# Optimization experiments

Hardware: AMD Instinct MI355X
Metric: run time of the kernel (lower is better)

The kernel has to match this reference:

```python
import jax, jax.numpy as jnp
import numpy as np
from jax.scipy.special import logsumexp

N_STATES = 512
N_OBS = 1024
BATCH = 64
T_MAX = 512


def setup_inputs() -> dict:
    key = jax.random.key(0)
    k1, k2, k3, k4, k5 = jax.random.split(key, 5)
    pi = jnp.zeros((N_STATES,), dtype=jnp.float32)
    A = jax.random.normal(k1, (N_STATES, N_STATES), dtype=jnp.float32)  # unnormalized transition
    E = jax.random.normal(k2, (N_STATES, N_OBS), dtype=jnp.float32)     # unnormalized emission
    x = jax.random.randint(k3, (BATCH, T_MAX), 0, N_OBS)
    T = jax.random.randint(k4, (BATCH,), 1, T_MAX + 1)
    return {"pi": pi, "A": A, "E": E, "x": x, "T": T}


def reference(pi, A, E, x, T):
    # log p(x) via forward algorithm in log domain.
    log_pi = jax.nn.log_softmax(pi)                # (N,)
    log_A = jax.nn.log_softmax(A, axis=0)          # (N,N), matches torch dim=0
    log_E = jax.nn.log_softmax(E, axis=1)          # (N,M)

    # emission log-probs per timestep: (B, T_max, N)
    log_em = jnp.moveaxis(log_E[:, x], 0, -1)

    alpha0 = log_em[:, 0, :] + log_pi              # (B,N)

    def step(carry, em_t):
        # carry: (B,N) over k; log_A: (N_i, N_k)
        # next[b,i] = em_t[b,i] + logsumexp_k(log_A[i,k] + carry[b,k])
        nxt = em_t + logsumexp(log_A[None, :, :] + carry[:, None, :], axis=2)
        return nxt, nxt

    em_rest = jnp.swapaxes(log_em[:, 1:, :], 0, 1)  # (T_max-1, B, N)
    _, alphas = jax.lax.scan(step, alpha0, em_rest)
    log_alpha = jnp.concatenate([alpha0[:, None, :], jnp.swapaxes(alphas, 0, 1)], axis=1)  # (B,T_max,N)

    log_sums = logsumexp(log_alpha, axis=2)         # (B, T_max)
    log_probs = jnp.take_along_axis(log_sums, (T - 1)[:, None], axis=1)  # (B,1)
    return log_probs
```

## Files before the change

kernel.cpp:

```cpp
#include <hip/hip_runtime.h>
#include <math.h>

#define NS   512
#define NO   1024
#define NB   64
#define TMAX 512

#define QREG 50
#define QLDS 14

typedef _Float16 h2v __attribute__((ext_vector_type(2)));

__device__ inline float wave_red_sum(float x) {
#pragma unroll
  for (int o = 32; o; o >>= 1) x += __shfl_xor(x, o, 64);
  return x;
}
__device__ inline float wave_red_max(float x) {
#pragma unroll
  for (int o = 32; o; o >>= 1) x = fmaxf(x, __shfl_xor(x, o, 64));
  return x;
}

__device__ inline float dot2u(unsigned int a, unsigned int b, float c) {
#if __has_builtin(__builtin_amdgcn_fdot2)
  return __builtin_amdgcn_fdot2(__builtin_bit_cast(h2v, a),
                                __builtin_bit_cast(h2v, b), c, false);
#else
  h2v av = __builtin_bit_cast(h2v, a), bv = __builtin_bit_cast(h2v, b);
  return c + (float)av.x * (float)bv.x + (float)av.y * (float)bv.y;
#endif
}

__global__ void k_pi(const float* __restrict__ pi, float* __restrict__ pi_sm) {
  __shared__ float red[8];
  int tid = threadIdx.x;
  float v = pi[tid];
  float m = wave_red_max(v);
  if ((tid & 63) == 0) red[tid >> 6] = m;
  __syncthreads();
  m = fmaxf(fmaxf(fmaxf(red[0], red[1]), fmaxf(red[2], red[3])),
            fmaxf(fmaxf(red[4], red[5]), fmaxf(red[6], red[7])));
  float e = __expf(v - m);
  float s = wave_red_sum(e);
  __syncthreads();
  if ((tid & 63) == 0) red[tid >> 6] = s;
  __syncthreads();
  s = red[0] + red[1] + red[2] + red[3] + red[4] + red[5] + red[6] + red[7];
  pi_sm[tid] = e / s;
}

__global__ void k_colLse(const float* __restrict__ A, float* __restrict__ lseA) {
  __shared__ float redm[4];
  __shared__ float reds[4];
  int k = blockIdx.x, tid = threadIdx.x;
  float a0 = A[tid * NS + k], a1 = A[(tid + 256) * NS + k];
  float m = wave_red_max(fmaxf(a0, a1));
  if ((tid & 63) == 0) redm[tid >> 6] = m;
  __syncthreads();
  m = fmaxf(fmaxf(redm[0], redm[1]), fmaxf(redm[2], redm[3]));
  float s = __expf(a0 - m) + __expf(a1 - m);
  s = wave_red_sum(s);
  if ((tid & 63) == 0) reds[tid >> 6] = s;
  __syncthreads();
  s = reds[0] + reds[1] + reds[2] + reds[3];
  if (tid == 0) lseA[k] = m + __logf(s);
}

__global__ void k_rowLseE(const float* __restrict__ E, float* __restrict__ lseE) {
  __shared__ float red[4];
  int i = blockIdx.x, tid = threadIdx.x;
  const float* row = E + i * NO;
  float a0 = row[tid], a1 = row[tid + 256], a2 = row[tid + 512], a3 = row[tid + 768];
  float m = fmaxf(fmaxf(a0, a1), fmaxf(a2, a3));
  m = wave_red_max(m);
  if ((tid & 63) == 0) red[tid >> 6] = m;
  __syncthreads();
  m = fmaxf(fmaxf(red[0], red[1]), fmaxf(red[2], red[3]));
  float s = __expf(a0 - m) + __expf(a1 - m) + __expf(a2 - m) + __expf(a3 - m);
  s = wave_red_sum(s);
  __syncthreads();
  if ((tid & 63) == 0) red[tid >> 6] = s;
  __syncthreads();
  s = red[0] + red[1] + red[2] + red[3];
  if (tid == 0) lseE[i] = m + __logf(s);
}

__global__ void k_pack(const float* __restrict__ A, const float* __restrict__ lseA,
                       unsigned int* __restrict__ W) {
  int u = blockIdx.x * 512 + threadIdx.x;
  int h = u & 3;
  int ct = u >> 2;
  int t = ct & 511;
  int c = ct >> 9;
  int j = c >> 3, m = c & 7;
  int w = t >> 6, l = t & 63;
  int i  = 64 * j + l;
  int k0 = 64 * w + 8 * m + 2 * h;
  float e0 = __expf(A[i * NS + k0]     - lseA[k0]);
  float e1 = __expf(A[i * NS + k0 + 1] - lseA[k0 + 1]);
  h2v p;
  p.x = (_Float16)e0;
  p.y = (_Float16)e1;
  W[u] = __builtin_bit_cast(unsigned int, p);
}

__global__ __launch_bounds__(512, 1) void k_fwd(
    const float* __restrict__ E, const int* __restrict__ x,
    const int* __restrict__ Tlen, const float* __restrict__ pi_sm,
    const float* __restrict__ lseE, const uint4* __restrict__ Apk,
    float* __restrict__ out) {
  __shared__ uint4 Alds[QLDS * 512];
  __shared__ float Pf[2][8 * 512];
  __shared__ uint4 ubuf[NS / 8];
  __shared__ int xrow[TMAX];
  __shared__ __align__(16) float red[2][8];
  int b = blockIdx.x, tid = threadIdx.x;
  int w = tid >> 6, l = tid & 63;

  uint4 areg[QREG];
#pragma unroll
  for (int q = 0; q < QREG; q++) areg[q] = Apk[q * 512 + tid];
#pragma unroll
  for (int q = 0; q < QLDS; q++) Alds[q * 512 + tid] = Apk[(QREG + q) * 512 + tid];

  for (int t2 = tid; t2 < TMAX; t2 += 512) xrow[t2] = x[b * TMAX + t2];

  float pi_i  = pi_sm[tid];
  float lse_i = lseE[tid];
  const float* Erow = E + tid * NO;
  int Tb = Tlen[b];
  float c = 0.f;
  float Dlog = 0.f;
  int gexp_prev = 19;
  int cur = 0;
  __syncthreads();

  for (int t = 0; t < Tb; t++) {
    int nxt = cur ^ 1;
    float epre = Erow[xrow[t]];
    if (t) {
      uint4 uv0 = ubuf[8 * w + 0], uv1 = ubuf[8 * w + 1];
      uint4 uv2 = ubuf[8 * w + 2], uv3 = ubuf[8 * w + 3];
      uint4 uv4 = ubuf[8 * w + 4], uv5 = ubuf[8 * w + 5];
      uint4 uv6 = ubuf[8 * w + 6], uv7 = ubuf[8 * w + 7];
      float acc[8];
#pragma unroll
      for (int j = 0; j < 8; j++) acc[j] = 0.f;
#pragma unroll
      for (int j = 0; j < 8; j++) {
#pragma unroll
        for (int m = 0; m < 8; m++) {
          int cq = j * 8 + m;
          uint4 av = (cq < QREG) ? areg[cq] : Alds[(cq - QREG) * 512 + tid];
          uint4 uv = (m == 0) ? uv0 : (m == 1) ? uv1 : (m == 2) ? uv2 :
                     (m == 3) ? uv3 : (m == 4) ? uv4 : (m == 5) ? uv5 :
                     (m == 6) ? uv6 : uv7;
          acc[j] = dot2u(av.x, uv.x, acc[j]);
          acc[j] = dot2u(av.y, uv.y, acc[j]);
          acc[j] = dot2u(av.z, uv.z, acc[j]);
          acc[j] = dot2u(av.w, uv.w, acc[j]);
        }
      }
#pragma unroll
      for (int j = 0; j < 8; j++) Pf[cur][w * 512 + j * 64 + l] = acc[j];
    }
    __syncthreads();

    {
      int gexpw = 19;
      if (t) {
        const float4* rp = (const float4*)red[cur];
        float4 ra = rp[0], rb = rp[1];
        float sp = ((ra.x + ra.y) + (ra.z + ra.w)) + ((rb.x + rb.y) + (rb.z + rb.w));
        float ls = __log2f(sp);
        int e = ((__builtin_bit_cast(int, sp) >> 23) & 0xff) - 126;
        c += ls - Dlog;
        Dlog = (float)gexp_prev + ls;
        gexpw = 19 - gexp_prev - e;
      }
      float em = __expf(epre - lse_i);
      float raw;
      if (t) {
        const float* pf = Pf[cur];
        float s0 = pf[tid]          + pf[512 + tid];
        float s1 = pf[1024 + tid]   + pf[1536 + tid];
        float s2 = pf[2048 + tid]   + pf[2560 + tid];
        float s3 = pf[3072 + tid]   + pf[3584 + tid];
        raw = ((s0 + s1) + (s2 + s3)) * em;
      } else {
        raw = pi_i * em;
      }
      ((_Float16*)ubuf)[tid] = (_Float16)ldexpf(raw, gexpw);
      float s = wave_red_sum(raw);
      if (l == 0) red[nxt][w] = s;
      gexp_prev = gexpw;
    }
    cur = nxt;
  }
  __syncthreads();
  {
    const float4* rp = (const float4*)red[cur];
    float4 ra = rp[0], rb = rp[1];
    float sp = ((ra.x + ra.y) + (ra.z + ra.w)) + ((rb.x + rb.y) + (rb.z + rb.w));
    c += __log2f(sp) - Dlog;
  }
  if (tid == 0) out[b] = c * 0.69314718055994530942f;
}

extern "C" void kernel_launch(void* const* d_in, const int* in_sizes, int n_in,
                              void* d_out, int out_size, void* d_ws, size_t ws_size,
                              hipStream_t stream) {
  const float* pi = (const float*)d_in[0];
  const float* A  = (const float*)d_in[1];
  const float* E  = (const float*)d_in[2];
  const int*   x  = (const int*)d_in[3];
  const int*   T  = (const int*)d_in[4];
  float* out = (float*)d_out;

  char* ws = (char*)d_ws;
  float*        pi_sm = (float*)(ws + 0);
  float*        lseA  = (float*)(ws + 2048);
  float*        lseE  = (float*)(ws + 4096);
  unsigned int* Apk   = (unsigned int*)(ws + 6144);

  hipLaunchKernelGGL(k_pi,      dim3(1),   dim3(512), 0, stream, pi, pi_sm);
  hipLaunchKernelGGL(k_colLse,  dim3(512), dim3(256), 0, stream, A, lseA);
  hipLaunchKernelGGL(k_rowLseE, dim3(512), dim3(256), 0, stream, E, lseE);
  hipLaunchKernelGGL(k_pack,    dim3(256), dim3(512), 0, stream, A, lseA, Apk);
  hipLaunchKernelGGL(k_fwd,     dim3(64),  dim3(512), 0, stream,
                     E, x, T, pi_sm, lseE, (const uint4*)Apk, out);
}
```

Measured before the change: 833.3 us.

## Store transition matrix as FP8 e5m2 and expand to fp16 for dot2

Packs the normalized transition probabilities into 8-bit e5m2 (scaled by 256) instead of fp16, halving the per-block storage of A so that fewer uint4s are held in registers and LDS. In the forward loop each byte pair is expanded to fp16 with a byte permute before the fdot2, and the 1/256 scale is folded into the emission multiply. This trades a couple of extra ALU ops per dot for reduced register pressure and LDS traffic, at the cost of much coarser precision (2-bit mantissa) on the transition weights, which may hurt accuracy.

```diff
diff --git a/kernel.cpp b/kernel.cpp
--- a/kernel.cpp
+++ b/kernel.cpp
@@ -6,8 +6,8 @@
 #define NB   64
 #define TMAX 512
 
-#define QREG 50
-#define QLDS 14
+#define QREG8 19
+#define QLDS8 13
 
 typedef _Float16 h2v __attribute__((ext_vector_type(2)));
 
@@ -32,6 +32,27 @@
 #endif
 }
 
+__device__ inline unsigned int ex_lo(unsigned int w) {
+#if __has_builtin(__builtin_amdgcn_perm)
+  return __builtin_amdgcn_perm(0u, w, 0x010C000Cu);
+#else
+  return ((w & 0xFFu) << 8) | ((w & 0xFF00u) << 16);
+#endif
+}
+__device__ inline unsigned int ex_hi(unsigned int w) {
+#if __has_builtin(__builtin_amdgcn_perm)
+  return __builtin_amdgcn_perm(0u, w, 0x030C020Cu);
+#else
+  return ((w & 0x00FF0000u) >> 8) | (w & 0xFF000000u);
+#endif
+}
+
+__device__ inline unsigned int f2e5m2(float f) {
+  unsigned short hb = __builtin_bit_cast(unsigned short, (_Float16)f);
+  unsigned int r = (unsigned int)hb + 0x7Fu + ((hb >> 8) & 1u);
+  return (r >> 8) & 0xFFu;
+}
+
 __global__ void k_pi(const float* __restrict__ pi, float* __restrict__ pi_sm) {
   __shared__ float red[8];
   int tid = threadIdx.x;
@@ -92,17 +113,17 @@
   int h = u & 3;
   int ct = u >> 2;
   int t = ct & 511;
-  int c = ct >> 9;
-  int j = c >> 3, m = c & 7;
+  int c8 = ct >> 9;
+  int j = c8 >> 2, n = c8 & 3;
   int w = t >> 6, l = t & 63;
   int i  = 64 * j + l;
-  int k0 = 64 * w + 8 * m + 2 * h;
-  float e0 = __expf(A[i * NS + k0]     - lseA[k0]);
-  float e1 = __expf(A[i * NS + k0 + 1] - lseA[k0 + 1]);
-  h2v p;
-  p.x = (_Float16)e0;
-  p.y = (_Float16)e1;
-  W[u] = __builtin_bit_cast(unsigned int, p);
+  int k0 = 64 * w + 16 * n + 4 * h;
+  const float* row = A + i * NS;
+  unsigned int b0 = f2e5m2(__expf(row[k0]     - lseA[k0])     * 256.f);
+  unsigned int b1 = f2e5m2(__expf(row[k0 + 1] - lseA[k0 + 1]) * 256.f);
+  unsigned int b2 = f2e5m2(__expf(row[k0 + 2] - lseA[k0 + 2]) * 256.f);
+  unsigned int b3 = f2e5m2(__expf(row[k0 + 3] - lseA[k0 + 3]) * 256.f);
+  W[u] = b0 | (b1 << 8) | (b2 << 16) | (b3 << 24);
 }
 
 __global__ __launch_bounds__(512, 1) void k_fwd(
@@ -110,7 +131,7 @@
     const int* __restrict__ Tlen, const float* __restrict__ pi_sm,
     const float* __restrict__ lseE, const uint4* __restrict__ Apk,
     float* __restrict__ out) {
-  __shared__ uint4 Alds[QLDS * 512];
+  __shared__ uint4 Alds[QLDS8 * 512];
   __shared__ float Pf[2][8 * 512];
   __shared__ uint4 ubuf[NS / 8];
   __shared__ int xrow[TMAX];
@@ -118,11 +139,11 @@
   int b = blockIdx.x, tid = threadIdx.x;
   int w = tid >> 6, l = tid & 63;
 
-  uint4 areg[QREG];
-#pragma unroll
-  for (int q = 0; q < QREG; q++) areg[q] = Apk[q * 512 + tid];
-#pragma unroll
-  for (int q = 0; q < QLDS; q++) Alds[q * 512 + tid] = Apk[(QREG + q) * 512 + tid];
+  uint4 areg8[QREG8];
+#pragma unroll
+  for (int q = 0; q < QREG8; q++) areg8[q] = Apk[q * 512 + tid];
+#pragma unroll
+  for (int q = 0; q < QLDS8; q++) Alds[q * 512 + tid] = Apk[(QREG8 + q) * 512 + tid];
 
   for (int t2 = tid; t2 < TMAX; t2 += 512) xrow[t2] = x[b * TMAX + t2];
 
@@ -140,26 +161,29 @@
     int nxt = cur ^ 1;
     float epre = Erow[xrow[t]];
     if (t) {
-      uint4 uv0 = ubuf[8 * w + 0], uv1 = ubuf[8 * w + 1];
-      uint4 uv2 = ubuf[8 * w + 2], uv3 = ubuf[8 * w + 3];
-      uint4 uv4 = ubuf[8 * w + 4], uv5 = ubuf[8 * w + 5];
-      uint4 uv6 = ubuf[8 * w + 6], uv7 = ubuf[8 * w + 7];
+      uint4 uvA0 = ubuf[8 * w + 0], uvB0 = ubuf[8 * w + 1];
+      uint4 uvA1 = ubuf[8 * w + 2], uvB1 = ubuf[8 * w + 3];
+      uint4 uvA2 = ubuf[8 * w + 4], uvB2 = ubuf[8 * w + 5];
+      uint4 uvA3 = ubuf[8 * w + 6], uvB3 = ubuf[8 * w + 7];
       float acc[8];
 #pragma unroll
       for (int j = 0; j < 8; j++) acc[j] = 0.f;
 #pragma unroll
       for (int j = 0; j < 8; j++) {
 #pragma unroll
-        for (int m = 0; m < 8; m++) {
-          int cq = j * 8 + m;
-          uint4 av = (cq < QREG) ? areg[cq] : Alds[(cq - QREG) * 512 + tid];
-          uint4 uv = (m == 0) ? uv0 : (m == 1) ? uv1 : (m == 2) ? uv2 :
-                     (m == 3) ? uv3 : (m == 4) ? uv4 : (m == 5) ? uv5 :
-                     (m == 6) ? uv6 : uv7;
-          acc[j] = dot2u(av.x, uv.x, acc[j]);
-          acc[j] = dot2u(av.y, uv.y, acc[j]);
-          acc[j] = dot2u(av.z, uv.z, acc[j]);
-          acc[j] = dot2u(av.w, uv.w, acc[j]);
+        for (int n = 0; n < 4; n++) {
+          int c8 = j * 4 + n;
+          uint4 av = (c8 < QREG8) ? areg8[c8] : Alds[(c8 - QREG8) * 512 + tid];
+          uint4 uvA = (n == 0) ? uvA0 : (n == 1) ? uvA1 : (n == 2) ? uvA2 : uvA3;
+          uint4 uvB = (n == 0) ? uvB0 : (n == 1) ? uvB1 : (n == 2) ? uvB2 : uvB3;
+          acc[j] = dot2u(ex_lo(av.x), uvA.x, acc[j]);
+          acc[j] = dot2u(ex_hi(av.x), uvA.y, acc[j]);
+          acc[j] = dot2u(ex_lo(av.y), uvA.z, acc[j]);
+          acc[j] = dot2u(ex_hi(av.y), uvA.w, acc[j]);
+          acc[j] = dot2u(ex_lo(av.z), uvB.x, acc[j]);
+          acc[j] = dot2u(ex_hi(av.z), uvB.y, acc[j]);
+          acc[j] = dot2u(ex_lo(av.w), uvB.z, acc[j]);
+          acc[j] = dot2u(ex_hi(av.w), uvB.w, acc[j]);
         }
       }
 #pragma unroll
@@ -187,7 +211,7 @@
         float s1 = pf[1024 + tid]   + pf[1536 + tid];
         float s2 = pf[2048 + tid]   + pf[2560 + tid];
         float s3 = pf[3072 + tid]   + pf[3584 + tid];
-        raw = ((s0 + s1) + (s2 + s3)) * em;
+        raw = ((s0 + s1) + (s2 + s3)) * (em * 0.00390625f);
       } else {
         raw = pi_i * em;
       }
@@ -227,7 +251,7 @@
   hipLaunchKernelGGL(k_pi,      dim3(1),   dim3(512), 0, stream, pi, pi_sm);
   hipLaunchKernelGGL(k_colLse,  dim3(512), dim3(256), 0, stream, A, lseA);
   hipLaunchKernelGGL(k_rowLseE, dim3(512), dim3(256), 0, stream, E, lseE);
-  hipLaunchKernelGGL(k_pack,    dim3(256), dim3(512), 0, stream, A, lseA, Apk);
+  hipLaunchKernelGGL(k_pack,    dim3(128), dim3(512), 0, stream, A, lseA, Apk);
   hipLaunchKernelGGL(k_fwd,     dim3(64),  dim3(512), 0, stream,
                      E, x, T, pi_sm, lseE, (const uint4*)Apk, out);
 }
```

Measured after the change: 1.063 ms. 27.6% more time.

## Double threads per batch block in forward recursion and halve per-thread K slice

Applied to the files above, without the earlier changes.

The forward-kernel block grows from 512 to 1024 threads. Each wave now covers a 32-wide slice of the previous-state dimension instead of 64, so each thread's register and LDS share of the packed transition matrix halves and the dot-product chain per step is shorter. Partial sums go through LDS as packed fp16 pairs. Only half the lanes own a state for the emission, normalisation and reduction phase. This is meant to cut the serial per-step latency, at the cost of fp16 rounding in the partial sums, idle lanes in the epilogue and heavier barriers.

```diff
diff --git a/kernel.cpp b/kernel.cpp
--- a/kernel.cpp
+++ b/kernel.cpp
@@ -6,8 +6,8 @@
 #define NB   64
 #define TMAX 512
 
-#define QREG 50
-#define QLDS 14
+#define QREG 25
+#define QLDS 7
 
 typedef _Float16 h2v __attribute__((ext_vector_type(2)));
 
@@ -91,12 +91,12 @@
   int u = blockIdx.x * 512 + threadIdx.x;
   int h = u & 3;
   int ct = u >> 2;
-  int t = ct & 511;
-  int c = ct >> 9;
-  int j = c >> 3, m = c & 7;
+  int t = ct & 1023;
+  int c = ct >> 10;
+  int j = c >> 2, n = c & 3;
   int w = t >> 6, l = t & 63;
   int i  = 64 * j + l;
-  int k0 = 64 * w + 8 * m + 2 * h;
+  int k0 = 32 * w + 8 * n + 2 * h;
   float e0 = __expf(A[i * NS + k0]     - lseA[k0]);
   float e1 = __expf(A[i * NS + k0 + 1] - lseA[k0 + 1]);
   h2v p;
@@ -105,30 +105,37 @@
   W[u] = __builtin_bit_cast(unsigned int, p);
 }
 
-__global__ __launch_bounds__(512, 1) void k_fwd(
+__global__ __launch_bounds__(1024, 1) void k_fwd(
     const float* __restrict__ E, const int* __restrict__ x,
     const int* __restrict__ Tlen, const float* __restrict__ pi_sm,
     const float* __restrict__ lseE, const uint4* __restrict__ Apk,
     float* __restrict__ out) {
-  __shared__ uint4 Alds[QLDS * 512];
-  __shared__ float Pf[2][8 * 512];
-  __shared__ uint4 ubuf[NS / 8];
+  __shared__ uint4 Alds[QLDS * 1024];
+  __shared__ unsigned int Pf[2][8 * 512];
+  __shared__ __align__(16) uint4 ubuf[NS / 8];
   __shared__ int xrow[TMAX];
-  __shared__ __align__(16) float red[2][8];
+  __shared__ __align__(16) float red[2][16];
   int b = blockIdx.x, tid = threadIdx.x;
   int w = tid >> 6, l = tid & 63;
+  int lo = l & 31;
+  bool owner = (l < 32);
+  int i_own = 32 * w + lo;
 
   uint4 areg[QREG];
 #pragma unroll
-  for (int q = 0; q < QREG; q++) areg[q] = Apk[q * 512 + tid];
-#pragma unroll
-  for (int q = 0; q < QLDS; q++) Alds[q * 512 + tid] = Apk[(QREG + q) * 512 + tid];
-
-  for (int t2 = tid; t2 < TMAX; t2 += 512) xrow[t2] = x[b * TMAX + t2];
-
-  float pi_i  = pi_sm[tid];
-  float lse_i = lseE[tid];
-  const float* Erow = E + tid * NO;
+  for (int q = 0; q < QREG; q++) areg[q] = Apk[q * 1024 + tid];
+#pragma unroll
+  for (int q = 0; q < QLDS; q++) Alds[q * 1024 + tid] = Apk[(QREG + q) * 1024 + tid];
+
+  for (int t2 = tid; t2 < TMAX; t2 += 1024) xrow[t2] = x[b * TMAX + t2];
+
+  float pi_i = 0.f, lse_i = 0.f;
+  const float* Erow = E;
+  if (owner) {
+    pi_i  = pi_sm[i_own];
+    lse_i = lseE[i_own];
+    Erow  = E + i_own * NO;
+  }
   int Tb = Tlen[b];
   float c = 0.f;
   float Dlog = 0.f;
@@ -138,32 +145,30 @@
 
   for (int t = 0; t < Tb; t++) {
     int nxt = cur ^ 1;
-    float epre = Erow[xrow[t]];
+    float epre = owner ? Erow[xrow[t]] : 0.f;
     if (t) {
-      uint4 uv0 = ubuf[8 * w + 0], uv1 = ubuf[8 * w + 1];
-      uint4 uv2 = ubuf[8 * w + 2], uv3 = ubuf[8 * w + 3];
-      uint4 uv4 = ubuf[8 * w + 4], uv5 = ubuf[8 * w + 5];
-      uint4 uv6 = ubuf[8 * w + 6], uv7 = ubuf[8 * w + 7];
+      uint4 uv0 = ubuf[4 * w + 0], uv1 = ubuf[4 * w + 1];
+      uint4 uv2 = ubuf[4 * w + 2], uv3 = ubuf[4 * w + 3];
       float acc[8];
 #pragma unroll
       for (int j = 0; j < 8; j++) acc[j] = 0.f;
 #pragma unroll
       for (int j = 0; j < 8; j++) {
 #pragma unroll
-        for (int m = 0; m < 8; m++) {
-          int cq = j * 8 + m;
-          uint4 av = (cq < QREG) ? areg[cq] : Alds[(cq - QREG) * 512 + tid];
-          uint4 uv = (m == 0) ? uv0 : (m == 1) ? uv1 : (m == 2) ? uv2 :
-                     (m == 3) ? uv3 : (m == 4) ? uv4 : (m == 5) ? uv5 :
-                     (m == 6) ? uv6 : uv7;
+        for (int n = 0; n < 4; n++) {
+          int cq = j * 4 + n;
+          uint4 av = (cq < QREG) ? areg[cq] : Alds[(cq - QREG) * 1024 + tid];
+          uint4 uv = (n == 0) ? uv0 : (n == 1) ? uv1 : (n == 2) ? uv2 : uv3;
           acc[j] = dot2u(av.x, uv.x, acc[j]);
           acc[j] = dot2u(av.y, uv.y, acc[j]);
           acc[j] = dot2u(av.z, uv.z, acc[j]);
           acc[j] = dot2u(av.w, uv.w, acc[j]);
         }
       }
-#pragma unroll
-      for (int j = 0; j < 8; j++) Pf[cur][w * 512 + j * 64 + l] = acc[j];
+      _Float16* pfh = (_Float16*)Pf[cur];
+#pragma unroll
+      for (int j = 0; j < 8; j++)
+        pfh[(((w >> 1) * 512 + 64 * j + l) << 1) | (w & 1)] = (_Float16)acc[j];
     }
     __syncthreads();
 
@@ -171,29 +176,39 @@
       int gexpw = 19;
       if (t) {
         const float4* rp = (const float4*)red[cur];
-        float4 ra = rp[0], rb = rp[1];
-        float sp = ((ra.x + ra.y) + (ra.z + ra.w)) + ((rb.x + rb.y) + (rb.z + rb.w));
+        float4 r0 = rp[0], r1 = rp[1], r2 = rp[2], r3 = rp[3];
+        float sp = (((r0.x + r0.y) + (r0.z + r0.w)) + ((r1.x + r1.y) + (r1.z + r1.w)))
+                 + (((r2.x + r2.y) + (r2.z + r2.w)) + ((r3.x + r3.y) + (r3.z + r3.w)));
         float ls = __log2f(sp);
         int e = ((__builtin_bit_cast(int, sp) >> 23) & 0xff) - 126;
         c += ls - Dlog;
         Dlog = (float)gexp_prev + ls;
         gexpw = 19 - gexp_prev - e;
       }
-      float em = __expf(epre - lse_i);
-      float raw;
-      if (t) {
-        const float* pf = Pf[cur];
-        float s0 = pf[tid]          + pf[512 + tid];
-        float s1 = pf[1024 + tid]   + pf[1536 + tid];
-        float s2 = pf[2048 + tid]   + pf[2560 + tid];
-        float s3 = pf[3072 + tid]   + pf[3584 + tid];
-        raw = ((s0 + s1) + (s2 + s3)) * em;
-      } else {
-        raw = pi_i * em;
+      if (owner) {
+        float em = __expf(epre - lse_i);
+        float raw;
+        if (t) {
+          const unsigned int* pf = Pf[cur];
+          float ssum = 0.f;
+#pragma unroll
+          for (int kk2 = 0; kk2 < 8; kk2++) {
+            h2v pv = __builtin_bit_cast(h2v, pf[kk2 * 512 + i_own]);
+            ssum += (float)pv.x + (float)pv.y;
+          }
+          raw = ssum * em;
+        } else {
+          raw = pi_i * em;
+        }
+        ((_Float16*)ubuf)[i_own] = (_Float16)ldexpf(raw, gexpw);
+        float s = raw;
+        s += __shfl_xor(s, 16, 64);
+        s += __shfl_xor(s, 8, 64);
+        s += __shfl_xor(s, 4, 64);
+        s += __shfl_xor(s, 2, 64);
+        s += __shfl_xor(s, 1, 64);
+        if (lo == 0) red[nxt][w] = s;
       }
-      ((_Float16*)ubuf)[tid] = (_Float16)ldexpf(raw, gexpw);
-      float s = wave_red_sum(raw);
-      if (l == 0) red[nxt][w] = s;
       gexp_prev = gexpw;
     }
     cur = nxt;
@@ -201,8 +216,9 @@
   __syncthreads();
   {
     const float4* rp = (const float4*)red[cur];
-    float4 ra = rp[0], rb = rp[1];
-    float sp = ((ra.x + ra.y) + (ra.z + ra.w)) + ((rb.x + rb.y) + (rb.z + rb.w));
+    float4 r0 = rp[0], r1 = rp[1], r2 = rp[2], r3 = rp[3];
+    float sp = (((r0.x + r0.y) + (r0.z + r0.w)) + ((r1.x + r1.y) + (r1.z + r1.w)))
+             + (((r2.x + r2.y) + (r2.z + r2.w)) + ((r3.x + r3.y) + (r3.z + r3.w)));
     c += __log2f(sp) - Dlog;
   }
   if (tid == 0) out[b] = c * 0.69314718055994530942f;
@@ -224,10 +240,10 @@
   float*        lseE  = (float*)(ws + 4096);
   unsigned int* Apk   = (unsigned int*)(ws + 6144);
 
-  hipLaunchKernelGGL(k_pi,      dim3(1),   dim3(512), 0, stream, pi, pi_sm);
-  hipLaunchKernelGGL(k_colLse,  dim3(512), dim3(256), 0, stream, A, lseA);
-  hipLaunchKernelGGL(k_rowLseE, dim3(512), dim3(256), 0, stream, E, lseE);
-  hipLaunchKernelGGL(k_pack,    dim3(256), dim3(512), 0, stream, A, lseA, Apk);
-  hipLaunchKernelGGL(k_fwd,     dim3(64),  dim3(512), 0, stream,
+  hipLaunchKernelGGL(k_pi,      dim3(1),   dim3(512),  0, stream, pi, pi_sm);
+  hipLaunchKernelGGL(k_colLse,  dim3(512), dim3(256),  0, stream, A, lseA);
+  hipLaunchKernelGGL(k_rowLseE, dim3(512), dim3(256),  0, stream, E, lseE);
+  hipLaunchKernelGGL(k_pack,    dim3(256), dim3(512),  0, stream, A, lseA, Apk);
+  hipLaunchKernelGGL(k_fwd,     dim3(64),  dim3(1024), 0, stream,
                      E, x, T, pi_sm, lseE, (const uint4*)Apk, out);
 }
```

Result: slower. 1.212 ms (+45.5%).
